# Performance work log

Hardware: AMD Instinct MI355X
Metric: run time of the kernel (lower is better)

## Reference

```python
import jax, jax.numpy as jnp
import numpy as np

DIM = 1024
D_STATE = 16
D_CONV = 4
EXPAND = 2
D_INNER = EXPAND * DIM
BATCH = 4
SEQ = 2048


def setup_inputs() -> dict:
    key = jax.random.key(0)
    ks = jax.random.split(key, 9)
    n = lambda i, shape, scale=0.02: (jax.random.normal(ks[i], shape, jnp.float32) * scale)
    return {
        "x": jax.random.normal(ks[0], (BATCH, SEQ, DIM), jnp.float32),
        "in_proj_w": n(1, (D_INNER, DIM)),
        "conv_w": n(2, (D_INNER, D_CONV), 0.1),          # depthwise kernel (groups=d_inner)
        "x_proj_w": n(3, (2 * D_STATE + 1, D_INNER)),
        "dt_proj_w": n(4, (D_INNER, 1), 1.0),
        "dt_proj_b": n(5, (D_INNER,), 0.1),
        "A_log": jax.random.normal(ks[6], (D_INNER, D_STATE), jnp.float32),
        "D": jnp.ones((D_INNER,), jnp.float32),
        "out_proj_w": n(7, (DIM, D_INNER)),
        "norm_w": jnp.ones((DIM,), jnp.float32),
        "norm_b": jnp.zeros((DIM,), jnp.float32),
    }


def reference(x, in_proj_w, conv_w, x_proj_w, dt_proj_w, dt_proj_b,
              A_log, D, out_proj_w, norm_w, norm_b):
    Bsz, L, _ = x.shape
    shortcut = x

    # LayerNorm
    mu = jnp.mean(x, axis=-1, keepdims=True)
    var = jnp.var(x, axis=-1, keepdims=True)
    h = (x - mu) / jnp.sqrt(var + 1e-5) * norm_w + norm_b

    # in_proj: [B,L,dim] -> [B,L,d_inner]
    h = h @ in_proj_w.T

    # causal depthwise conv1d (padding d_conv-1, truncate to L)
    hp = jnp.pad(h, ((0, 0), (D_CONV - 1, 0), (0, 0)))
    h_conv = sum(hp[:, k:k + L, :] * conv_w[:, k] for k in range(D_CONV))
    h = jax.nn.silu(h_conv)

    # x_proj -> dt (1), B (d_state), C (d_state)
    proj = h @ x_proj_w.T
    dt_in = proj[..., :1]
    B_param = proj[..., 1:1 + D_STATE]      # [B,L,d_state]
    C_param = proj[..., 1 + D_STATE:]       # [B,L,d_state]
    dt = jax.nn.softplus(dt_in @ dt_proj_w.T + dt_proj_b)  # [B,L,d_inner]

    A = -jnp.exp(A_log)                     # [d_inner, d_state]

    def step(state, inp):
        dt_t, B_t, C_t, x_t = inp           # [B,d_inner],[B,ds],[B,ds],[B,d_inner]
        state = jnp.exp(A[None] * dt_t[:, :, None]) * state \
                + B_t[:, None, :] * x_t[:, :, None]          # [B,d_inner,d_state]
        y = jnp.einsum('bnd,bd->bn', state, C_t) + D * x_t   # [B,d_inner]
        return state, y

    init = jnp.zeros((Bsz, D_INNER, D_STATE), x.dtype)
    xs = (jnp.swapaxes(dt, 0, 1), jnp.swapaxes(B_param, 0, 1),
          jnp.swapaxes(C_param, 0, 1), jnp.swapaxes(h, 0, 1))
    state, ys = jax.lax.scan(step, init, xs)
    y = jnp.swapaxes(ys, 0, 1)              # [B,L,d_inner]

    out = jax.nn.silu(y) @ out_proj_w.T + shortcut
    return out, state
```

## Files before the change

### kernel.cpp

```cpp
#include <hip/hip_runtime.h>

typedef unsigned short u16;
typedef unsigned int u32;
typedef __attribute__((ext_vector_type(8))) short short8;
typedef __attribute__((ext_vector_type(4))) float f32x4;
typedef __attribute__((ext_vector_type(2))) float f32x2;
typedef __attribute__((ext_vector_type(8))) unsigned short ushort8_t;

#define SEQ 2048
#define DIM 1024
#define DINNER 2048
#define NPROJ 33
#define NPROJ_PAD 48
#define LC 16
#define NC 128

__device__ __forceinline__ u16 f2bf(float f) {
  union { float f; u32 u; } v; v.f = f;
  u32 r = (v.u + 0x7fffu + ((v.u >> 16) & 1u)) >> 16;
  return (u16)r;
}
__device__ __forceinline__ float bf2f(u16 s) {
  union { u32 u; float f; } v; v.u = ((u32)s) << 16;
  return v.f;
}
__device__ __forceinline__ float lo_bf(u32 w) {
  union { u32 u; float f; } v; v.u = w << 16; return v.f;
}
__device__ __forceinline__ float hi_bf(u32 w) {
  union { u32 u; float f; } v; v.u = w & 0xffff0000u; return v.f;
}
__device__ __forceinline__ float fexp2(float x) {
#if __has_builtin(__builtin_amdgcn_exp2f)
  return __builtin_amdgcn_exp2f(x);
#else
  return __expf(x * 0.69314718f);
#endif
}
__device__ __forceinline__ float frcp(float x) {
#if __has_builtin(__builtin_amdgcn_rcpf)
  return __builtin_amdgcn_rcpf(x);
#else
  return 1.f / x;
#endif
}
__device__ __forceinline__ float softplus(float x) {
  return fmaxf(x, 0.f) + __logf(1.f + __expf(-fabsf(x)));
}
__device__ __forceinline__ f32x2 sp2(float v) { f32x2 r; r.x = v; r.y = v; return r; }
__device__ __forceinline__ f32x2 pkfma(f32x2 a, f32x2 b, f32x2 c) {
  return __builtin_elementwise_fma(a, b, c);
}
__device__ __forceinline__ void async16(const void* g, void* l) {
  __builtin_amdgcn_global_load_lds(
      (const __attribute__((address_space(1))) u32*)g,
      (__attribute__((address_space(3))) u32*)l, 16, 0, 0);
}

__global__ void cast_w_kernel(const float* __restrict__ w1, const float* __restrict__ w3,
                              u16* __restrict__ o1, u16* __restrict__ o3) {
  int i = blockIdx.x * 256 + threadIdx.x;
  float4 a = ((const float4*)w1)[i];
  float4 b = ((const float4*)w3)[i];
  ushort4 oa, ob;
  oa.x = f2bf(a.x); oa.y = f2bf(a.y); oa.z = f2bf(a.z); oa.w = f2bf(a.w);
  ob.x = f2bf(b.x); ob.y = f2bf(b.y); ob.z = f2bf(b.z); ob.w = f2bf(b.w);
  ((ushort4*)o1)[i] = oa;
  ((ushort4*)o3)[i] = ob;
}

__global__ void cast_w2pad_kernel(const float* __restrict__ src, u16* __restrict__ dst) {
  int i = blockIdx.x * 256 + threadIdx.x;
  int j = i >> 11, k = i & 2047;
  u16 v;
  if (j < 32) v = f2bf(src[(1 + j) * 2048 + k]);
  else if (j == 32) v = f2bf(src[k]);
  else v = (u16)0;
  dst[i] = v;
}

__global__ void foldA_kernel(const float* __restrict__ A_log, float* __restrict__ A2) {
  int i = blockIdx.x * 256 + threadIdx.x;
  int p = i >> 5, n2 = i & 31;
  int d = p * 2 + (n2 & 1), n = n2 >> 1;
  A2[i] = -__expf(A_log[d * 16 + n]) * 1.44269504f;
}

__global__ __launch_bounds__(256) void ln_kernel(const float* __restrict__ x,
                                                 const float* __restrict__ w,
                                                 const float* __restrict__ b,
                                                 u16* __restrict__ h) {
  const int row = blockIdx.x;
  const int tid = threadIdx.x;
  const int lane = tid & 63, wave = tid >> 6;
  const float4 v = ((const float4*)(x + (size_t)row * DIM))[tid];
  float s = v.x + v.y + v.z + v.w;
  float q = v.x * v.x + v.y * v.y + v.z * v.z + v.w * v.w;
  for (int off = 32; off; off >>= 1) {
    s += __shfl_down(s, off);
    q += __shfl_down(q, off);
  }
  __shared__ float sbuf[8];
  if (lane == 0) { sbuf[wave] = s; sbuf[4 + wave] = q; }
  __syncthreads();
  float tot = sbuf[0] + sbuf[1] + sbuf[2] + sbuf[3];
  float totq = sbuf[4] + sbuf[5] + sbuf[6] + sbuf[7];
  const float mean = tot * (1.0f / DIM);
  const float var = totq * (1.0f / DIM) - mean * mean;
  const float rs = rsqrtf(var + 1e-5f);
  const float4 wv = ((const float4*)w)[tid];
  const float4 bv = ((const float4*)b)[tid];
  ushort4 o;
  o.x = f2bf((v.x - mean) * rs * wv.x + bv.x);
  o.y = f2bf((v.y - mean) * rs * wv.y + bv.y);
  o.z = f2bf((v.z - mean) * rs * wv.z + bv.z);
  o.w = f2bf((v.w - mean) * rs * wv.w + bv.w);
  ((ushort4*)(h + (size_t)row * DIM))[tid] = o;
}

__global__ __launch_bounds__(512) void gemm_bf16_kernel(const u16* __restrict__ A,
                                                        const u16* __restrict__ Bt,
                                                        u16* __restrict__ C,
                                                        int K, int N) {
  __shared__ u16 As[128 * 32];
  __shared__ u16 Bs[128 * 32];
  const int tid = threadIdx.x;
  const int lane = tid & 63, wave = tid >> 6;
  const int wm = wave >> 2, wn = wave & 3;
  const int row16 = lane & 15, quad = lane >> 4;
  const int flat = blockIdx.x + gridDim.x * blockIdx.y;
  const int xcd = flat & 7;
  const int sidx = flat >> 3;
  const int bm = xcd * 8 + (sidx & 7);
  const int bn = sidx >> 3;
  f32x4 acc[4][2] = {};
  const u16* Ablk = A + (size_t)bm * 128 * K;
  const u16* Bblk = Bt + (size_t)bn * 128 * K;
  const int r = tid >> 2, cc = (tid & 3) * 8;
  for (int k0 = 0; k0 < K; k0 += 32) {
    async16(Ablk + (size_t)r * K + k0 + cc, &As[tid * 8]);
    async16(Bblk + (size_t)r * K + k0 + cc, &Bs[tid * 8]);
    __syncthreads();
    short8 af[4], bfr[2];
#pragma unroll
    for (int i = 0; i < 4; ++i)
      af[i] = *(const short8*)&As[(wm * 64 + i * 16 + row16) * 32 + quad * 8];
#pragma unroll
    for (int j = 0; j < 2; ++j)
      bfr[j] = *(const short8*)&Bs[(wn * 32 + j * 16 + row16) * 32 + quad * 8];
#pragma unroll
    for (int i = 0; i < 4; ++i)
#pragma unroll
      for (int j = 0; j < 2; ++j)
        acc[i][j] = __builtin_amdgcn_mfma_f32_16x16x32_bf16(af[i], bfr[j], acc[i][j], 0, 0, 0);
    __syncthreads();
  }
#pragma unroll
  for (int i = 0; i < 4; ++i) {
    int m = bm * 128 + wm * 64 + i * 16 + quad * 4;
#pragma unroll
    for (int j = 0; j < 2; ++j) {
      int n = bn * 128 + wn * 32 + j * 16 + row16;
#pragma unroll
      for (int rr = 0; rr < 4; ++rr)
        C[(size_t)(m + rr) * N + n] = f2bf(acc[i][j][rr]);
    }
  }
}

__global__ __launch_bounds__(512) void gemm_out_kernel(const u16* __restrict__ A,
                                                       const u16* __restrict__ Bt,
                                                       const float* __restrict__ resid,
                                                       float* __restrict__ C,
                                                       int K, int N) {
  __shared__ u16 As[128 * 32];
  __shared__ u16 Bs[128 * 32];
  const int tid = threadIdx.x;
  const int lane = tid & 63, wave = tid >> 6;
  const int wm = wave >> 2, wn = wave & 3;
  const int row16 = lane & 15, quad = lane >> 4;
  const int flat = blockIdx.x + gridDim.x * blockIdx.y;
  const int xcd = flat & 7;
  const int sidx = flat >> 3;
  const int bm = xcd * 8 + (sidx & 7);
  const int bn = sidx >> 3;
  f32x4 acc[4][2] = {};
  const u16* Ablk = A + (size_t)bm * 128 * K;
  const u16* Bblk = Bt + (size_t)bn * 128 * K;
  const int r = tid >> 2, cc = (tid & 3) * 8;
  for (int k0 = 0; k0 < K; k0 += 32) {
    async16(Ablk + (size_t)r * K + k0 + cc, &As[tid * 8]);
    async16(Bblk + (size_t)r * K + k0 + cc, &Bs[tid * 8]);
    __syncthreads();
    short8 af[4], bfr[2];
#pragma unroll
    for (int i = 0; i < 4; ++i)
      af[i] = *(const short8*)&As[(wm * 64 + i * 16 + row16) * 32 + quad * 8];
#pragma unroll
    for (int j = 0; j < 2; ++j)
      bfr[j] = *(const short8*)&Bs[(wn * 32 + j * 16 + row16) * 32 + quad * 8];
#pragma unroll
    for (int i = 0; i < 4; ++i)
#pragma unroll
      for (int j = 0; j < 2; ++j)
        acc[i][j] = __builtin_amdgcn_mfma_f32_16x16x32_bf16(af[i], bfr[j], acc[i][j], 0, 0, 0);
    __syncthreads();
  }
#pragma unroll
  for (int i = 0; i < 4; ++i) {
    int m = bm * 128 + wm * 64 + i * 16 + quad * 4;
#pragma unroll
    for (int j = 0; j < 2; ++j) {
      int n = bn * 128 + wn * 32 + j * 16 + row16;
#pragma unroll
      for (int rr = 0; rr < 4; ++rr) {
        size_t idx = (size_t)(m + rr) * N + n;
        C[idx] = acc[i][j][rr] + resid[idx];
      }
    }
  }
}

__global__ __launch_bounds__(256) void conv_silu_kernel(const u16* __restrict__ c1,
                                                        const float* __restrict__ cw,
                                                        u16* __restrict__ cs) {
  const int tid = threadIdx.x;
  const int dg = tid * 8;
  const size_t m0 = (size_t)blockIdx.x * 8;
  const int l0 = (int)(m0 & (SEQ - 1));
  float w[4][8];
  {
    const float4* cw4 = (const float4*)(cw + (size_t)dg * 4);
#pragma unroll
    for (int c = 0; c < 8; ++c) {
      float4 v = cw4[c];
      w[0][c] = v.x; w[1][c] = v.y; w[2][c] = v.z; w[3][c] = v.w;
    }
  }
  const u16* base = c1 + m0 * DINNER + dg;
  ushort8_t win0, win1, win2, win3;
  const ushort8_t zero = (ushort8_t)0;
  if (l0 == 0) {
    win0 = zero; win1 = zero; win2 = zero;
  } else {
    win0 = *(const ushort8_t*)(base - 3 * DINNER);
    win1 = *(const ushort8_t*)(base - 2 * DINNER);
    win2 = *(const ushort8_t*)(base - 1 * DINNER);
  }
  win3 = *(const ushort8_t*)(base);
#pragma unroll
  for (int t = 0; t < 8; ++t) {
    ushort8_t nxt = win3;
    if (t < 7) nxt = *(const ushort8_t*)(base + (size_t)(t + 1) * DINNER);
    ushort8_t o;
#pragma unroll
    for (int c = 0; c < 8; ++c) {
      float acc = bf2f((u16)win0[c]) * w[0][c];
      acc = fmaf(bf2f((u16)win1[c]), w[1][c], acc);
      acc = fmaf(bf2f((u16)win2[c]), w[2][c], acc);
      acc = fmaf(bf2f((u16)win3[c]), w[3][c], acc);
      const float s = acc * frcp(1.f + __expf(-acc));
      o[c] = (unsigned short)f2bf(s);
    }
    *(ushort8_t*)(cs + (m0 + t) * DINNER + dg) = o;
    win0 = win1; win1 = win2; win2 = win3; win3 = nxt;
  }
}

__global__ __launch_bounds__(128) void gemm_w2_kernel(const u16* __restrict__ A,
                                                      const u16* __restrict__ Bt,
                                                      float* __restrict__ C) {
  __shared__ u16 As[32 * 32];
  __shared__ u16 Bs[48 * 32];
  const int tid = threadIdx.x;
  const int lane = tid & 63, wave = tid >> 6;
  const int row16 = lane & 15, quad = lane >> 4;
  const int bm = blockIdx.x;
  const int K = DINNER;
  f32x4 acc[3] = {};
  const u16* Ablk = A + (size_t)bm * 32 * K;
  const int r = tid >> 2, cc = (tid & 3) * 8;
  for (int k0 = 0; k0 < K; k0 += 32) {
    async16(Ablk + (size_t)r * K + k0 + cc, &As[tid * 8]);
    async16(Bt + (size_t)r * K + k0 + cc, &Bs[tid * 8]);
    if (tid < 64)
      async16(Bt + (size_t)(32 + r) * K + k0 + cc, &Bs[1024 + tid * 8]);
    __syncthreads();
    short8 af = *(const short8*)&As[(wave * 16 + row16) * 32 + quad * 8];
    short8 bfr[3];
#pragma unroll
    for (int j = 0; j < 3; ++j)
      bfr[j] = *(const short8*)&Bs[(j * 16 + row16) * 32 + quad * 8];
#pragma unroll
    for (int j = 0; j < 3; ++j)
      acc[j] = __builtin_amdgcn_mfma_f32_16x16x32_bf16(af, bfr[j], acc[j], 0, 0, 0);
    __syncthreads();
  }
  const int m = bm * 32 + wave * 16 + quad * 4;
#pragma unroll
  for (int j = 0; j < 3; ++j) {
    const int n = j * 16 + row16;
#pragma unroll
    for (int rr = 0; rr < 4; ++rr)
      C[(size_t)(m + rr) * NPROJ_PAD + n] = acc[j][rr];
  }
}


__global__ __launch_bounds__(256) void scan_phase1(const float* __restrict__ proj,
                                                   const u16* __restrict__ xs,
                                                   const float* __restrict__ dtw_,
                                                   const float* __restrict__ dtb_,
                                                   const float* __restrict__ A2,
                                                   u16* __restrict__ S,
                                                   float* __restrict__ Tdt) {
  const int tid = threadIdx.x;
  const int d0 = blockIdx.x * 512 + tid * 2;
  const int c = blockIdx.y;
  const int b = blockIdx.z;
  const size_t mrow = (size_t)b * SEQ + c * LC;
  f32x2 An2[16];
  {
    const float4* Ap = (const float4*)(A2 + (size_t)(d0 >> 1) * 32);
#pragma unroll
    for (int q = 0; q < 8; ++q) {
      float4 v = Ap[q];
      An2[2 * q].x = v.x;     An2[2 * q].y = v.y;
      An2[2 * q + 1].x = v.z; An2[2 * q + 1].y = v.w;
    }
  }
  const float2 dtwv = *(const float2*)(dtw_ + d0);
  const float2 dtbv = *(const float2*)(dtb_ + d0);
  f32x2 dtw2; dtw2.x = dtwv.x; dtw2.y = dtwv.y;
  f32x2 dtb2; dtb2.x = dtbv.x; dtb2.y = dtbv.y;
  f32x2 s[16];
#pragma unroll
  for (int n = 0; n < 16; ++n) s[n] = sp2(0.f);
  f32x2 Tsum = sp2(0.f);
  const float* pr = proj + mrow * NPROJ_PAD;
  const u16* xp = xs + mrow * DINNER + d0;
  u32 xw = *(const u32*)xp;
#pragma unroll 2
  for (int t = 0; t < LC; ++t) {
    f32x2 xv; xv.x = lo_bf(xw); xv.y = hi_bf(xw);
    if (t + 1 < LC) xw = *(const u32*)(xp + (size_t)(t + 1) * DINNER);
    const float dtin = pr[32];
    f32x2 dtv = pkfma(sp2(dtin), dtw2, dtb2);
    f32x2 sp; sp.x = softplus(dtv.x); sp.y = softplus(dtv.y);
    Tsum += sp;
    const float4* Br = (const float4*)pr;
#pragma unroll
    for (int q = 0; q < 4; ++q) {
      const float4 Bq = Br[q];
      const float bqa[4] = {Bq.x, Bq.y, Bq.z, Bq.w};
#pragma unroll
      for (int j = 0; j < 4; ++j) {
        const int n = q * 4 + j;
        f32x2 e = An2[n] * sp;
        f32x2 dk; dk.x = fexp2(e.x); dk.y = fexp2(e.y);
        s[n] = pkfma(dk, s[n], sp2(bqa[j]) * xv);
      }
    }
    pr += NPROJ_PAD;
  }
  const size_t so = ((size_t)(b * NC + c) * DINNER + d0) * 16;
  ushort8_t o0, o1, o2, o3;
#pragma unroll
  for (int j = 0; j < 8; ++j) {
    o0[j] = f2bf(s[j].x);     o1[j] = f2bf(s[8 + j].x);
    o2[j] = f2bf(s[j].y);     o3[j] = f2bf(s[8 + j].y);
  }
  *(ushort8_t*)(S + so) = o0;       *(ushort8_t*)(S + so + 8) = o1;
  *(ushort8_t*)(S + so + 16) = o2;  *(ushort8_t*)(S + so + 24) = o3;
  *(float2*)(Tdt + (size_t)(b * NC + c) * DINNER + d0) = make_float2(Tsum.x, Tsum.y);
}

__global__ __launch_bounds__(256) void scan_phase2(const float* __restrict__ A2,
                                                   u16* __restrict__ S,
                                                   const float* __restrict__ Tdt,
                                                   float* __restrict__ out_state) {
  const int idx = blockIdx.x * 256 + threadIdx.x;
  const int n = idx & 15;
  const int d = (idx >> 4) & (DINNER - 1);
  const int b = idx >> 15;
  const float An = A2[((d >> 1) << 5) + (n << 1) + (d & 1)];
  float prev = 0.f;
#pragma unroll 4
  for (int c = 0; c < NC; ++c) {
    const size_t base = (size_t)(b * NC + c) * DINNER + d;
    const float T = Tdt[base];
    const size_t so = base * 16 + n;
    const float loc = bf2f(S[so]);
    S[so] = f2bf(prev);
    prev = fmaf(fexp2(An * T), prev, loc);
  }
  out_state[((size_t)b * DINNER + d) * 16 + n] = prev;
}

__global__ __launch_bounds__(256) void scan_phase3(const float* __restrict__ proj,
                                                   const u16* __restrict__ xs,
                                                   const float* __restrict__ dtw_,
                                                   const float* __restrict__ dtb_,
                                                   const float* __restrict__ A2,
                                                   const float* __restrict__ Dp,
                                                   const u16* __restrict__ S,
                                                   u16* __restrict__ ysil) {
  const int tid = threadIdx.x;
  const int d0 = blockIdx.x * 512 + tid * 2;
  const int c = blockIdx.y;
  const int b = blockIdx.z;
  const size_t mrow = (size_t)b * SEQ + c * LC;
  f32x2 An2[16];
  {
    const float4* Ap = (const float4*)(A2 + (size_t)(d0 >> 1) * 32);
#pragma unroll
    for (int q = 0; q < 8; ++q) {
      float4 v = Ap[q];
      An2[2 * q].x = v.x;     An2[2 * q].y = v.y;
      An2[2 * q + 1].x = v.z; An2[2 * q + 1].y = v.w;
    }
  }
  const float2 dtwv = *(const float2*)(dtw_ + d0);
  const float2 dtbv = *(const float2*)(dtb_ + d0);
  const float2 Ddv = *(const float2*)(Dp + d0);
  f32x2 dtw2; dtw2.x = dtwv.x; dtw2.y = dtwv.y;
  f32x2 dtb2; dtb2.x = dtbv.x; dtb2.y = dtbv.y;
  f32x2 Dd2; Dd2.x = Ddv.x; Dd2.y = Ddv.y;
  f32x2 s[16];
  const size_t so = ((size_t)(b * NC + c) * DINNER + d0) * 16;
  {
    ushort8_t v0 = *(const ushort8_t*)(S + so);
    ushort8_t v1 = *(const ushort8_t*)(S + so + 8);
    ushort8_t v2 = *(const ushort8_t*)(S + so + 16);
    ushort8_t v3 = *(const ushort8_t*)(S + so + 24);
#pragma unroll
    for (int j = 0; j < 8; ++j) {
      s[j].x = bf2f((u16)v0[j]);     s[8 + j].x = bf2f((u16)v1[j]);
      s[j].y = bf2f((u16)v2[j]);     s[8 + j].y = bf2f((u16)v3[j]);
    }
  }
  const float* pr = proj + mrow * NPROJ_PAD;
  const u16* xp = xs + mrow * DINNER + d0;
  u16* yp = ysil + mrow * DINNER + d0;
  u32 xw = *(const u32*)xp;
#pragma unroll 2
  for (int t = 0; t < LC; ++t) {
    f32x2 xv; xv.x = lo_bf(xw); xv.y = hi_bf(xw);
    if (t + 1 < LC) xw = *(const u32*)(xp + (size_t)(t + 1) * DINNER);
    const float dtin = pr[32];
    f32x2 dtv = pkfma(sp2(dtin), dtw2, dtb2);
    f32x2 sp; sp.x = softplus(dtv.x); sp.y = softplus(dtv.y);
    f32x2 y = Dd2 * xv;
    const float4* Br = (const float4*)pr;
    const float4* Cr = (const float4*)(pr + 16);
#pragma unroll
    for (int q = 0; q < 4; ++q) {
      const float4 Bq = Br[q];
      const float4 Cq = Cr[q];
      const float bqa[4] = {Bq.x, Bq.y, Bq.z, Bq.w};
      const float cqa[4] = {Cq.x, Cq.y, Cq.z, Cq.w};
#pragma unroll
      for (int j = 0; j < 4; ++j) {
        const int n = q * 4 + j;
        f32x2 e = An2[n] * sp;
        f32x2 dk; dk.x = fexp2(e.x); dk.y = fexp2(e.y);
        s[n] = pkfma(dk, s[n], sp2(bqa[j]) * xv);
        y = pkfma(sp2(cqa[j]), s[n], y);
      }
    }
    const float sy0 = y.x * frcp(1.f + __expf(-y.x));
    const float sy1 = y.y * frcp(1.f + __expf(-y.y));
    const u32 ow = (u32)f2bf(sy0) | ((u32)f2bf(sy1) << 16);
    *(u32*)(yp + (size_t)t * DINNER) = ow;
    pr += NPROJ_PAD;
  }
}

extern "C" void kernel_launch(void* const* d_in, const int* in_sizes, int n_in,
                              void* d_out, int out_size, void* d_ws, size_t ws_size,
                              hipStream_t stream) {
  const float* x = (const float*)d_in[0];
  const float* in_proj_w = (const float*)d_in[1];
  const float* conv_w = (const float*)d_in[2];
  const float* x_proj_w = (const float*)d_in[3];
  const float* dt_proj_w = (const float*)d_in[4];
  const float* dt_proj_b = (const float*)d_in[5];
  const float* A_log = (const float*)d_in[6];
  const float* Dvec = (const float*)d_in[7];
  const float* out_proj_w = (const float*)d_in[8];
  const float* norm_w = (const float*)d_in[9];
  const float* norm_b = (const float*)d_in[10];

  char* ws = (char*)d_ws;
  u16* h = (u16*)(ws + 0);
  u16* w1b = (u16*)(ws + 16777216);
  u16* w3b = (u16*)(ws + 20971520);
  u16* w2b = (u16*)(ws + 25165824);
  u16* c1 = (u16*)(ws + 25362432);
  u16* ysil = c1;
  u16* cs = (u16*)(ws + 58916864);
  float* proj = (float*)(ws + 92471296);
  float* Tdt = (float*)(ws + 94044160);
  float* A2 = (float*)(ws + 98238464);

  float* out = (float*)d_out;
  float* out_state = out + (size_t)4 * SEQ * DIM;
  u16* Sbuf = (u16*)d_out;

  cast_w_kernel<<<2048, 256, 0, stream>>>(in_proj_w, out_proj_w, w1b, w3b);
  cast_w2pad_kernel<<<384, 256, 0, stream>>>(x_proj_w, w2b);
  foldA_kernel<<<128, 256, 0, stream>>>(A_log, A2);
  ln_kernel<<<8192, 256, 0, stream>>>(x, norm_w, norm_b, h);
  gemm_bf16_kernel<<<dim3(DINNER / 128, 64), 512, 0, stream>>>(h, w1b, c1, DIM, DINNER);
  conv_silu_kernel<<<1024, 256, 0, stream>>>(c1, conv_w, cs);
  gemm_w2_kernel<<<256, 128, 0, stream>>>(cs, w2b, proj);
  scan_phase1<<<dim3(DINNER / 512, NC, 4), 256, 0, stream>>>(proj, cs, dt_proj_w, dt_proj_b,
                                                             A2, Sbuf, Tdt);
  scan_phase2<<<512, 256, 0, stream>>>(A2, Sbuf, Tdt, out_state);
  scan_phase3<<<dim3(DINNER / 512, NC, 4), 256, 0, stream>>>(proj, cs, dt_proj_w, dt_proj_b,
                                                             A2, Dvec, Sbuf, ysil);
  gemm_out_kernel<<<dim3(DIM / 128, 64), 512, 0, stream>>>(ysil, w3b, x, out, DINNER, DIM);
}
```

Before: 369.4 us.

## Merge prep kernels, use packed bf16 converts, split y accumulation in scan

Folds the three weight-cast and A-fold kernels into one prep kernel to cut launch overhead. Uses the hardware v_cvt_pk_bf16_f32 instruction for state and output stores, and unpacks loaded state with shifts. Raises scan-loop unroll from 2 to 4 and splits the C·state reduction into four partial accumulators to shorten the dependency chain. These add register pressure and may slightly change rounding, since the hardware convert and the reordered sum can differ from the previous software path.

```diff
diff --git a/kernel.cpp b/kernel.cpp
--- a/kernel.cpp
+++ b/kernel.cpp
@@ -30,6 +30,11 @@
 __device__ __forceinline__ float hi_bf(u32 w) {
   union { u32 u; float f; } v; v.u = w & 0xffff0000u; return v.f;
 }
+__device__ __forceinline__ u32 pkbf(float a, float b) {
+  u32 r;
+  asm("v_cvt_pk_bf16_f32 %0, %1, %2" : "=v"(r) : "v"(a), "v"(b));
+  return r;
+}
 __device__ __forceinline__ float fexp2(float x) {
 #if __has_builtin(__builtin_amdgcn_exp2f)
   return __builtin_amdgcn_exp2f(x);
@@ -57,33 +62,39 @@
       (__attribute__((address_space(3))) u32*)l, 16, 0, 0);
 }
 
-__global__ void cast_w_kernel(const float* __restrict__ w1, const float* __restrict__ w3,
-                              u16* __restrict__ o1, u16* __restrict__ o3) {
-  int i = blockIdx.x * 256 + threadIdx.x;
-  float4 a = ((const float4*)w1)[i];
-  float4 b = ((const float4*)w3)[i];
-  ushort4 oa, ob;
-  oa.x = f2bf(a.x); oa.y = f2bf(a.y); oa.z = f2bf(a.z); oa.w = f2bf(a.w);
-  ob.x = f2bf(b.x); ob.y = f2bf(b.y); ob.z = f2bf(b.z); ob.w = f2bf(b.w);
-  ((ushort4*)o1)[i] = oa;
-  ((ushort4*)o3)[i] = ob;
-}
-
-__global__ void cast_w2pad_kernel(const float* __restrict__ src, u16* __restrict__ dst) {
-  int i = blockIdx.x * 256 + threadIdx.x;
-  int j = i >> 11, k = i & 2047;
-  u16 v;
-  if (j < 32) v = f2bf(src[(1 + j) * 2048 + k]);
-  else if (j == 32) v = f2bf(src[k]);
-  else v = (u16)0;
-  dst[i] = v;
-}
-
-__global__ void foldA_kernel(const float* __restrict__ A_log, float* __restrict__ A2) {
-  int i = blockIdx.x * 256 + threadIdx.x;
-  int p = i >> 5, n2 = i & 31;
-  int d = p * 2 + (n2 & 1), n = n2 >> 1;
-  A2[i] = -__expf(A_log[d * 16 + n]) * 1.44269504f;
+__global__ __launch_bounds__(256) void prep_kernel(const float* __restrict__ w1,
+                                                   const float* __restrict__ w3,
+                                                   const float* __restrict__ xpw,
+                                                   const float* __restrict__ A_log,
+                                                   u16* __restrict__ o1,
+                                                   u16* __restrict__ o3,
+                                                   u16* __restrict__ w2b,
+                                                   float* __restrict__ A2) {
+  const int gb = blockIdx.x;
+  const int tid = threadIdx.x;
+  if (gb < 2048) {
+    int i = gb * 256 + tid;
+    float4 a = ((const float4*)w1)[i];
+    float4 b = ((const float4*)w3)[i];
+    ushort4 oa, ob;
+    oa.x = f2bf(a.x); oa.y = f2bf(a.y); oa.z = f2bf(a.z); oa.w = f2bf(a.w);
+    ob.x = f2bf(b.x); ob.y = f2bf(b.y); ob.z = f2bf(b.z); ob.w = f2bf(b.w);
+    ((ushort4*)o1)[i] = oa;
+    ((ushort4*)o3)[i] = ob;
+  } else if (gb < 2432) {
+    int i = (gb - 2048) * 256 + tid;
+    int j = i >> 11, k = i & 2047;
+    u16 v;
+    if (j < 32) v = f2bf(xpw[(1 + j) * 2048 + k]);
+    else if (j == 32) v = f2bf(xpw[k]);
+    else v = (u16)0;
+    w2b[i] = v;
+  } else {
+    int i = (gb - 2432) * 256 + tid;
+    int p = i >> 5, n2 = i & 31;
+    int d = p * 2 + (n2 & 1), n = n2 >> 1;
+    A2[i] = -__expf(A_log[d * 16 + n]) * 1.44269504f;
+  }
 }
 
 __global__ __launch_bounds__(256) void ln_kernel(const float* __restrict__ x,
@@ -340,7 +351,7 @@
   const float* pr = proj + mrow * NPROJ_PAD;
   const u16* xp = xs + mrow * DINNER + d0;
   u32 xw = *(const u32*)xp;
-#pragma unroll 2
+#pragma unroll 4
   for (int t = 0; t < LC; ++t) {
     f32x2 xv; xv.x = lo_bf(xw); xv.y = hi_bf(xw);
     if (t + 1 < LC) xw = *(const u32*)(xp + (size_t)(t + 1) * DINNER);
@@ -364,14 +375,17 @@
     pr += NPROJ_PAD;
   }
   const size_t so = ((size_t)(b * NC + c) * DINNER + d0) * 16;
-  ushort8_t o0, o1, o2, o3;
-#pragma unroll
-  for (int j = 0; j < 8; ++j) {
-    o0[j] = f2bf(s[j].x);     o1[j] = f2bf(s[8 + j].x);
-    o2[j] = f2bf(s[j].y);     o3[j] = f2bf(s[8 + j].y);
-  }
-  *(ushort8_t*)(S + so) = o0;       *(ushort8_t*)(S + so + 8) = o1;
-  *(ushort8_t*)(S + so + 16) = o2;  *(ushort8_t*)(S + so + 24) = o3;
+  uint4 w0, w1, w2, w3;
+  w0.x = pkbf(s[0].x, s[1].x);   w0.y = pkbf(s[2].x, s[3].x);
+  w0.z = pkbf(s[4].x, s[5].x);   w0.w = pkbf(s[6].x, s[7].x);
+  w1.x = pkbf(s[8].x, s[9].x);   w1.y = pkbf(s[10].x, s[11].x);
+  w1.z = pkbf(s[12].x, s[13].x); w1.w = pkbf(s[14].x, s[15].x);
+  w2.x = pkbf(s[0].y, s[1].y);   w2.y = pkbf(s[2].y, s[3].y);
+  w2.z = pkbf(s[4].y, s[5].y);   w2.w = pkbf(s[6].y, s[7].y);
+  w3.x = pkbf(s[8].y, s[9].y);   w3.y = pkbf(s[10].y, s[11].y);
+  w3.z = pkbf(s[12].y, s[13].y); w3.w = pkbf(s[14].y, s[15].y);
+  *(uint4*)(S + so) = w0;        *(uint4*)(S + so + 8) = w1;
+  *(uint4*)(S + so + 16) = w2;   *(uint4*)(S + so + 24) = w3;
   *(float2*)(Tdt + (size_t)(b * NC + c) * DINNER + d0) = make_float2(Tsum.x, Tsum.y);
 }
 
@@ -429,28 +443,35 @@
   f32x2 s[16];
   const size_t so = ((size_t)(b * NC + c) * DINNER + d0) * 16;
   {
-    ushort8_t v0 = *(const ushort8_t*)(S + so);
-    ushort8_t v1 = *(const ushort8_t*)(S + so + 8);
-    ushort8_t v2 = *(const ushort8_t*)(S + so + 16);
-    ushort8_t v3 = *(const ushort8_t*)(S + so + 24);
-#pragma unroll
-    for (int j = 0; j < 8; ++j) {
-      s[j].x = bf2f((u16)v0[j]);     s[8 + j].x = bf2f((u16)v1[j]);
-      s[j].y = bf2f((u16)v2[j]);     s[8 + j].y = bf2f((u16)v3[j]);
+    uint4 v0 = *(const uint4*)(S + so);
+    uint4 v1 = *(const uint4*)(S + so + 8);
+    uint4 v2 = *(const uint4*)(S + so + 16);
+    uint4 v3 = *(const uint4*)(S + so + 24);
+    const u32 a0[4] = {v0.x, v0.y, v0.z, v0.w};
+    const u32 a1[4] = {v1.x, v1.y, v1.z, v1.w};
+    const u32 a2[4] = {v2.x, v2.y, v2.z, v2.w};
+    const u32 a3[4] = {v3.x, v3.y, v3.z, v3.w};
+#pragma unroll
+    for (int j = 0; j < 4; ++j) {
+      s[2 * j].x = lo_bf(a0[j]);     s[2 * j + 1].x = hi_bf(a0[j]);
+      s[8 + 2 * j].x = lo_bf(a1[j]); s[8 + 2 * j + 1].x = hi_bf(a1[j]);
+      s[2 * j].y = lo_bf(a2[j]);     s[2 * j + 1].y = hi_bf(a2[j]);
+      s[8 + 2 * j].y = lo_bf(a3[j]); s[8 + 2 * j + 1].y = hi_bf(a3[j]);
     }
   }
   const float* pr = proj + mrow * NPROJ_PAD;
   const u16* xp = xs + mrow * DINNER + d0;
   u16* yp = ysil + mrow * DINNER + d0;
   u32 xw = *(const u32*)xp;
-#pragma unroll 2
+#pragma unroll 4
   for (int t = 0; t < LC; ++t) {
     f32x2 xv; xv.x = lo_bf(xw); xv.y = hi_bf(xw);
     if (t + 1 < LC) xw = *(const u32*)(xp + (size_t)(t + 1) * DINNER);
     const float dtin = pr[32];
     f32x2 dtv = pkfma(sp2(dtin), dtw2, dtb2);
     f32x2 sp; sp.x = softplus(dtv.x); sp.y = softplus(dtv.y);
-    f32x2 y = Dd2 * xv;
+    f32x2 ya[4];
+    ya[0] = Dd2 * xv; ya[1] = sp2(0.f); ya[2] = sp2(0.f); ya[3] = sp2(0.f);
     const float4* Br = (const float4*)pr;
     const float4* Cr = (const float4*)(pr + 16);
 #pragma unroll
@@ -465,13 +486,13 @@
         f32x2 e = An2[n] * sp;
         f32x2 dk; dk.x = fexp2(e.x); dk.y = fexp2(e.y);
         s[n] = pkfma(dk, s[n], sp2(bqa[j]) * xv);
-        y = pkfma(sp2(cqa[j]), s[n], y);
+        ya[q] = pkfma(sp2(cqa[j]), s[n], ya[q]);
       }
     }
+    f32x2 y = (ya[0] + ya[1]) + (ya[2] + ya[3]);
     const float sy0 = y.x * frcp(1.f + __expf(-y.x));
     const float sy1 = y.y * frcp(1.f + __expf(-y.y));
-    const u32 ow = (u32)f2bf(sy0) | ((u32)f2bf(sy1) << 16);
-    *(u32*)(yp + (size_t)t * DINNER) = ow;
+    *(u32*)(yp + (size_t)t * DINNER) = pkbf(sy0, sy1);
     pr += NPROJ_PAD;
   }
 }
@@ -507,9 +528,8 @@
   float* out_state = out + (size_t)4 * SEQ * DIM;
   u16* Sbuf = (u16*)d_out;
 
-  cast_w_kernel<<<2048, 256, 0, stream>>>(in_proj_w, out_proj_w, w1b, w3b);
-  cast_w2pad_kernel<<<384, 256, 0, stream>>>(x_proj_w, w2b);
-  foldA_kernel<<<128, 256, 0, stream>>>(A_log, A2);
+  prep_kernel<<<2560, 256, 0, stream>>>(in_proj_w, out_proj_w, x_proj_w, A_log,
+                                        w1b, w3b, w2b, A2);
   ln_kernel<<<8192, 256, 0, stream>>>(x, norm_w, norm_b, h);
   gemm_bf16_kernel<<<dim3(DINNER / 128, 64), 512, 0, stream>>>(h, w1b, c1, DIM, DINNER);
   conv_silu_kernel<<<1024, 256, 0, stream>>>(c1, conv_w, cs);
```

Result: faster. 358.9 us (-2.8%).
